# Optimization experiments

Measured on AMD Instinct MI355X. Metric: run time of the kernel, lower is better.

Reference implementation:

```python
import jax, jax.numpy as jnp
import numpy as np

B, N, E, H, F = 4, 10000, 100000, 8, 32
FIN = H * F  # num_in_features == H*F so skip connection is identity add


def setup_inputs() -> dict:
    key = jax.random.key(0)
    ks = jax.random.split(key, 6)
    x = jax.random.normal(ks[0], (B, N, FIN), jnp.float32)
    edge_index = jax.random.randint(ks[1], (B, 2, E), 0, N)
    rel = jax.random.normal(ks[2], (B, E, FIN), jnp.float32)
    W_proj = jax.random.normal(ks[3], (FIN, FIN), jnp.float32) / np.sqrt(FIN).astype(np.float32)
    a_src = jax.random.normal(ks[4], (1, H, F), jnp.float32) * 0.1
    a_trg = jax.random.normal(ks[5], (1, H, F), jnp.float32) * 0.1
    bias = jnp.zeros((FIN,), jnp.float32)
    return dict(x=x, edge_index=edge_index, rel=rel, W_proj=W_proj,
                a_src=a_src, a_trg=a_trg, bias=bias)


def reference(x, edge_index, rel, W_proj, a_src, a_trg, bias):
    # projection: [B,N,FIN] @ [FIN,FIN]^T -> [B,N,H,F]
    proj = (x @ W_proj.T).reshape(B, N, H, F)
    s_src = (proj * a_src).sum(-1)  # [B,N,H]
    s_trg = (proj * a_trg).sum(-1)  # [B,N,H]
    src, trg = edge_index[:, 0], edge_index[:, 1]  # [B,E] each

    gather = jax.vmap(lambda a, i: a[i])  # per-batch index_select along node dim

    # edge lift + leaky relu score: [B,E,H]
    s_e = jax.nn.leaky_relu(gather(s_src, src) + gather(s_trg, trg), negative_slope=0.2)
    # original subtracts the GLOBAL max per batch (over flattened E*H)
    s_e = s_e - s_e.reshape(B, -1).max(axis=-1)[:, None, None]
    exp_s = jnp.exp(s_e)

    # scatter softmax denominator over target-node neighborhoods
    seg_sum = jax.vmap(lambda s, t: jax.ops.segment_sum(s, t, num_segments=N))
    denom = seg_sum(exp_s, trg)               # [B,N,H]
    att = exp_s / (gather(denom, trg) + 1e-16)  # [B,E,H]

    # weighted messages + relation features projected with the same linear
    rel_proj = (rel @ W_proj.T).reshape(B, E, H, F)
    msg = gather(proj, src) * att[..., None] + rel_proj  # [B,E,H,F]

    # scatter-add aggregation to target nodes
    out = seg_sum(msg, trg)                   # [B,N,H,F]

    # skip connection (identity because FIN == H*F), concat heads, bias, ELU
    out = out + x.reshape(B, N, H, F)
    out = out.reshape(B, N, H * F) + bias
    return jax.nn.elu(out)
```

## Files before the change

kernel.cpp:

```cpp
#include <hip/hip_runtime.h>

#define B_ 4
#define N_ 10000
#define E_ 100000
#define H_ 8
#define F_ 32
#define FIN_ 256
#define M_ (B_*N_)
#define BE_ (B_*E_)

__device__ __forceinline__ unsigned enc_f(float f){
  unsigned u = __float_as_uint(f);
  return (u & 0x80000000u) ? ~u : (u | 0x80000000u);
}
__device__ __forceinline__ float dec_f(unsigned e){
  return (e & 0x80000000u) ? __uint_as_float(e & 0x7FFFFFFFu)
                           : __uint_as_float(~e);
}

template<int MODE>
__global__ __launch_bounds__(256)
void gemm_k(const float* __restrict__ A, const float* __restrict__ W,
            float* __restrict__ C,
            const float* __restrict__ add1, const float* __restrict__ add2,
            const float* __restrict__ bias)
{
  __shared__ float As[16][132];
  __shared__ float Bs[16][132];
  const int tid  = threadIdx.x;
  const int row0 = blockIdx.x * 128;
  const int col0 = blockIdx.y * 128;
  const int lr   = tid >> 2;
  const int lc4  = (tid & 3) * 4;
  const int tm   = (tid >> 4) * 8;
  const int tn   = (tid & 15) * 8;

  float acc[8][8];
  #pragma unroll
  for (int i = 0; i < 8; i++)
    #pragma unroll
    for (int j = 0; j < 8; j++) acc[i][j] = 0.f;

  for (int kt = 0; kt < FIN_; kt += 16) {
    #pragma unroll
    for (int half = 0; half < 2; half++) {
      int r = row0 + lr + half * 64;
      float4 v = make_float4(0.f, 0.f, 0.f, 0.f);
      if (r < M_) v = *(const float4*)&A[(size_t)r * FIN_ + kt + lc4];
      As[lc4+0][lr + half*64] = v.x;
      As[lc4+1][lr + half*64] = v.y;
      As[lc4+2][lr + half*64] = v.z;
      As[lc4+3][lr + half*64] = v.w;

      int j = col0 + lr + half * 64;
      float4 w = *(const float4*)&W[(size_t)j * FIN_ + kt + lc4];
      Bs[lc4+0][lr + half*64] = w.x;
      Bs[lc4+1][lr + half*64] = w.y;
      Bs[lc4+2][lr + half*64] = w.z;
      Bs[lc4+3][lr + half*64] = w.w;
    }
    __syncthreads();
    #pragma unroll
    for (int k = 0; k < 16; k++) {
      float a[8], b[8];
      *(float4*)&a[0] = *(const float4*)&As[k][tm];
      *(float4*)&a[4] = *(const float4*)&As[k][tm+4];
      *(float4*)&b[0] = *(const float4*)&Bs[k][tn];
      *(float4*)&b[4] = *(const float4*)&Bs[k][tn+4];
      #pragma unroll
      for (int i = 0; i < 8; i++)
        #pragma unroll
        for (int j = 0; j < 8; j++)
          acc[i][j] = fmaf(a[i], b[j], acc[i][j]);
    }
    __syncthreads();
  }

  #pragma unroll
  for (int i = 0; i < 8; i++) {
    int r = row0 + tm + i;
    if (r >= M_) continue;
    if (MODE == 0) {
      *(float4*)&C[(size_t)r * FIN_ + col0 + tn]     = *(float4*)&acc[i][0];
      *(float4*)&C[(size_t)r * FIN_ + col0 + tn + 4] = *(float4*)&acc[i][4];
    } else {
      #pragma unroll
      for (int j = 0; j < 8; j++) {
        int c = col0 + tn + j;
        float v = acc[i][j] + add1[(size_t)r * FIN_ + c]
                            + add2[(size_t)r * FIN_ + c] + bias[c];
        C[(size_t)r * FIN_ + c] = (v > 0.f) ? v : expm1f(v);
      }
    }
  }
}

__global__ void node_scores_k(const float* __restrict__ proj,
                              const float* __restrict__ a_src,
                              const float* __restrict__ a_trg,
                              float* __restrict__ s_src,
                              float* __restrict__ s_trg)
{
  int i = blockIdx.x * 256 + threadIdx.x;
  if (i >= M_ * H_) return;
  int h = i & 7;
  const float* p  = proj  + (size_t)i * F_;
  const float* as = a_src + h * F_;
  const float* at = a_trg + h * F_;
  float ss = 0.f, st = 0.f;
  #pragma unroll
  for (int f = 0; f < F_; f += 4) {
    float4 pv = *(const float4*)&p[f];
    float4 av = *(const float4*)&as[f];
    float4 tv = *(const float4*)&at[f];
    ss += pv.x*av.x + pv.y*av.y + pv.z*av.z + pv.w*av.w;
    st += pv.x*tv.x + pv.y*tv.y + pv.z*tv.z + pv.w*tv.w;
  }
  s_src[i] = ss;
  s_trg[i] = st;
}

__global__ void edge_scores_k(const int* __restrict__ ei,
                              const float* __restrict__ s_src,
                              const float* __restrict__ s_trg,
                              float* __restrict__ s_e,
                              unsigned* __restrict__ bmax)
{
  __shared__ unsigned smax[B_];
  if (threadIdx.x < B_) smax[threadIdx.x] = 0u;
  __syncthreads();

  int i = blockIdx.x * 256 + threadIdx.x;
  int b = 0;
  if (i < BE_) {
    b = i / E_;
    int e = i - b * E_;
    int src = ei[(size_t)b * 2 * E_ + e];
    int trg = ei[(size_t)b * 2 * E_ + E_ + e];
    const float* ps = s_src + ((size_t)b * N_ + src) * H_;
    const float* pt = s_trg + ((size_t)b * N_ + trg) * H_;
    float4 s0 = *(const float4*)ps,     s1 = *(const float4*)(ps + 4);
    float4 t0 = *(const float4*)pt,     t1 = *(const float4*)(pt + 4);
    float v[8] = { s0.x+t0.x, s0.y+t0.y, s0.z+t0.z, s0.w+t0.w,
                   s1.x+t1.x, s1.y+t1.y, s1.z+t1.z, s1.w+t1.w };
    float lmax = -3.4e38f;
    #pragma unroll
    for (int h = 0; h < 8; h++) {
      v[h] = (v[h] > 0.f) ? v[h] : 0.2f * v[h];
      lmax = fmaxf(lmax, v[h]);
    }
    *(float4*)&s_e[(size_t)i * 8]     = make_float4(v[0], v[1], v[2], v[3]);
    *(float4*)&s_e[(size_t)i * 8 + 4] = make_float4(v[4], v[5], v[6], v[7]);
    atomicMax(&smax[b], enc_f(lmax));
  }
  __syncthreads();
  if (threadIdx.x < B_ && smax[threadIdx.x] != 0u)
    atomicMax(&bmax[threadIdx.x], smax[threadIdx.x]);
}

__global__ void count_k(const int* __restrict__ ei, int* __restrict__ cnt)
{
  int i = blockIdx.x * 256 + threadIdx.x;
  if (i >= BE_) return;
  int b = i / E_, e = i - b * E_;
  int trg = ei[(size_t)b * 2 * E_ + E_ + e];
  atomicAdd(&cnt[b * N_ + trg], 1);
}

__global__ __launch_bounds__(1024)
void scan_k(const int* __restrict__ cnt, int* __restrict__ offs,
            int* __restrict__ cursor)
{
  int b = blockIdx.x;
  __shared__ int sdata[1024];
  __shared__ int carry;
  if (threadIdx.x == 0) carry = 0;
  __syncthreads();
  for (int base = 0; base < N_; base += 1024) {
    int idx = base + threadIdx.x;
    int v = (idx < N_) ? cnt[b * N_ + idx] : 0;
    sdata[threadIdx.x] = v;
    __syncthreads();
    #pragma unroll
    for (int off = 1; off < 1024; off <<= 1) {
      int t = (threadIdx.x >= off) ? sdata[threadIdx.x - off] : 0;
      __syncthreads();
      sdata[threadIdx.x] += t;
      __syncthreads();
    }
    int incl = sdata[threadIdx.x];
    int excl = incl - v + carry;
    if (idx < N_) {
      offs[b * N_ + idx]   = b * E_ + excl;
      cursor[b * N_ + idx] = b * E_ + excl;
    }
    __syncthreads();
    if (threadIdx.x == 1023) carry += incl;
    __syncthreads();
  }
}

__global__ void scatter_k(const int* __restrict__ ei, int* __restrict__ cursor,
                          int2* __restrict__ rec)
{
  int i = blockIdx.x * 256 + threadIdx.x;
  if (i >= BE_) return;
  int b = i / E_, e = i - b * E_;
  int src = ei[(size_t)b * 2 * E_ + e];
  int trg = ei[(size_t)b * 2 * E_ + E_ + e];
  int pos = atomicAdd(&cursor[b * N_ + trg], 1);
  rec[pos] = make_int2(src, i);
}

__global__ __launch_bounds__(256)
void agg_k(const int2* __restrict__ rec, const int* __restrict__ offs,
           const int* __restrict__ cnt, const float* __restrict__ s_e,
           const unsigned* __restrict__ bmax,
           const float* __restrict__ proj, const float* __restrict__ rel,
           float* __restrict__ rel_agg, float* __restrict__ out_acc)
{
  int node = blockIdx.x * 4 + (threadIdx.x >> 6);
  if (node >= M_) return;
  int lane = threadIdx.x & 63;
  int b = node / N_;
  float m = dec_f(bmax[b]);
  int start = offs[node];
  int num   = cnt[node];
  int h = lane >> 3;

  float4 pacc = make_float4(0.f, 0.f, 0.f, 0.f);
  float4 racc = make_float4(0.f, 0.f, 0.f, 0.f);
  float  dacc = 0.f;

  for (int i = 0; i < num; i++) {
    int2 r = rec[start + i];
    int src = r.x;
    int ge  = r.y;
    float ex = expf(s_e[(size_t)ge * 8 + h] - m);
    dacc += ex;
    float4 p = *(const float4*)&proj[((size_t)b * N_ + src) * FIN_ + lane * 4];
    pacc.x += p.x * ex; pacc.y += p.y * ex;
    pacc.z += p.z * ex; pacc.w += p.w * ex;
    float4 rv = *(const float4*)&rel[(size_t)ge * FIN_ + lane * 4];
    racc.x += rv.x; racc.y += rv.y; racc.z += rv.z; racc.w += rv.w;
  }

  float inv = 1.f / (dacc + 1e-16f);
  pacc.x *= inv; pacc.y *= inv; pacc.z *= inv; pacc.w *= inv;
  *(float4*)&out_acc[(size_t)node * FIN_ + lane * 4] = pacc;
  *(float4*)&rel_agg[(size_t)node * FIN_ + lane * 4] = racc;
}

extern "C" void kernel_launch(void* const* d_in, const int* in_sizes, int n_in,
                              void* d_out, int out_size, void* d_ws, size_t ws_size,
                              hipStream_t stream)
{
  const float* x     = (const float*)d_in[0];
  const int*   ei    = (const int*)  d_in[1];
  const float* rel   = (const float*)d_in[2];
  const float* W     = (const float*)d_in[3];
  const float* a_src = (const float*)d_in[4];
  const float* a_trg = (const float*)d_in[5];
  const float* bias  = (const float*)d_in[6];
  float* out = (float*)d_out;

  float* ws = (float*)d_ws;
  size_t o = 0;
  float* proj    = ws + o; o += (size_t)M_ * FIN_;
  float* s_src   = ws + o; o += (size_t)M_ * H_;
  float* s_trg   = ws + o; o += (size_t)M_ * H_;
  float* s_e     = ws + o; o += (size_t)BE_ * H_;
  float* rel_agg = ws + o; o += (size_t)M_ * FIN_;
  float* out_acc = ws + o; o += (size_t)M_ * FIN_;
  int* cnt       = (int*)(ws + o);      o += M_;
  unsigned* bmax = (unsigned*)(ws + o); o += B_;
  int* offs      = (int*)(ws + o);      o += M_;
  int* cursor    = (int*)(ws + o);      o += M_;
  if (o & 1) o++;
  int2* rec      = (int2*)(ws + o);     o += (size_t)2 * BE_;

  hipMemsetAsync(cnt, 0, (M_ + B_) * sizeof(int), stream);

  gemm_k<0><<<dim3(313, 2), 256, 0, stream>>>(x, W, proj, nullptr, nullptr, nullptr);

  node_scores_k<<<(M_ * H_ + 255) / 256, 256, 0, stream>>>(proj, a_src, a_trg, s_src, s_trg);

  edge_scores_k<<<(BE_ + 255) / 256, 256, 0, stream>>>(ei, s_src, s_trg, s_e, bmax);

  count_k<<<(BE_ + 255) / 256, 256, 0, stream>>>(ei, cnt);
  scan_k<<<B_, 1024, 0, stream>>>(cnt, offs, cursor);
  scatter_k<<<(BE_ + 255) / 256, 256, 0, stream>>>(ei, cursor, rec);

  agg_k<<<M_ / 4, 256, 0, stream>>>(rec, offs, cnt, s_e, bmax, proj, rel,
                                    rel_agg, out_acc);

  gemm_k<1><<<dim3(313, 2), 256, 0, stream>>>(rel_agg, W, out, out_acc, x, bias);
}
```

Measured before the change: 897.1 us.

## Swizzle GEMM LDS, vectorize epilogue, fuse count, single-block scan, prefetch agg records

```diff
diff --git a/kernel.cpp b/kernel.cpp
--- a/kernel.cpp
+++ b/kernel.cpp
@@ -9,6 +9,8 @@
 #define M_ (B_*N_)
 #define BE_ (B_*E_)
 
+typedef float f4 __attribute__((ext_vector_type(4)));
+
 __device__ __forceinline__ unsigned enc_f(float f){
   unsigned u = __float_as_uint(f);
   return (u & 0x80000000u) ? ~u : (u | 0x80000000u);
@@ -17,6 +19,8 @@
   return (e & 0x80000000u) ? __uint_as_float(e & 0x7FFFFFFFu)
                            : __uint_as_float(~e);
 }
+
+#define SW(c) ((c) + (((c) >> 5) << 1))
 
 template<int MODE>
 __global__ __launch_bounds__(256)
@@ -25,8 +29,8 @@
             const float* __restrict__ add1, const float* __restrict__ add2,
             const float* __restrict__ bias)
 {
-  __shared__ float As[16][132];
-  __shared__ float Bs[16][132];
+  __shared__ float As[16][136];
+  __shared__ float Bs[16][136];
   const int tid  = threadIdx.x;
   const int row0 = blockIdx.x * 128;
   const int col0 = blockIdx.y * 128;
@@ -44,29 +48,30 @@
   for (int kt = 0; kt < FIN_; kt += 16) {
     #pragma unroll
     for (int half = 0; half < 2; half++) {
-      int r = row0 + lr + half * 64;
+      int col = lr + half * 64;
+      int r = row0 + col;
       float4 v = make_float4(0.f, 0.f, 0.f, 0.f);
       if (r < M_) v = *(const float4*)&A[(size_t)r * FIN_ + kt + lc4];
-      As[lc4+0][lr + half*64] = v.x;
-      As[lc4+1][lr + half*64] = v.y;
-      As[lc4+2][lr + half*64] = v.z;
-      As[lc4+3][lr + half*64] = v.w;
-
-      int j = col0 + lr + half * 64;
+      As[lc4+0][SW(col)] = v.x;
+      As[lc4+1][SW(col)] = v.y;
+      As[lc4+2][SW(col)] = v.z;
+      As[lc4+3][SW(col)] = v.w;
+
+      int j = col0 + col;
       float4 w = *(const float4*)&W[(size_t)j * FIN_ + kt + lc4];
-      Bs[lc4+0][lr + half*64] = w.x;
-      Bs[lc4+1][lr + half*64] = w.y;
-      Bs[lc4+2][lr + half*64] = w.z;
-      Bs[lc4+3][lr + half*64] = w.w;
+      Bs[lc4+0][SW(col)] = w.x;
+      Bs[lc4+1][SW(col)] = w.y;
+      Bs[lc4+2][SW(col)] = w.z;
+      Bs[lc4+3][SW(col)] = w.w;
     }
     __syncthreads();
     #pragma unroll
     for (int k = 0; k < 16; k++) {
       float a[8], b[8];
-      *(float4*)&a[0] = *(const float4*)&As[k][tm];
-      *(float4*)&a[4] = *(const float4*)&As[k][tm+4];
-      *(float4*)&b[0] = *(const float4*)&Bs[k][tn];
-      *(float4*)&b[4] = *(const float4*)&Bs[k][tn+4];
+      *(float4*)&a[0] = *(const float4*)&As[k][SW(tm)];
+      *(float4*)&a[4] = *(const float4*)&As[k][SW(tm+4)];
+      *(float4*)&b[0] = *(const float4*)&Bs[k][SW(tn)];
+      *(float4*)&b[4] = *(const float4*)&Bs[k][SW(tn+4)];
       #pragma unroll
       for (int i = 0; i < 8; i++)
         #pragma unroll
@@ -84,12 +89,22 @@
       *(float4*)&C[(size_t)r * FIN_ + col0 + tn]     = *(float4*)&acc[i][0];
       *(float4*)&C[(size_t)r * FIN_ + col0 + tn + 4] = *(float4*)&acc[i][4];
     } else {
+      const size_t ro = (size_t)r * FIN_ + col0 + tn;
       #pragma unroll
-      for (int j = 0; j < 8; j++) {
-        int c = col0 + tn + j;
-        float v = acc[i][j] + add1[(size_t)r * FIN_ + c]
-                            + add2[(size_t)r * FIN_ + c] + bias[c];
-        C[(size_t)r * FIN_ + c] = (v > 0.f) ? v : expm1f(v);
+      for (int q = 0; q < 2; q++) {
+        float4 a1 = *(const float4*)&add1[ro + q*4];
+        float4 a2 = *(const float4*)&add2[ro + q*4];
+        float4 bb = *(const float4*)&bias[col0 + tn + q*4];
+        float vv[4] = { acc[i][q*4+0] + a1.x + a2.x + bb.x,
+                        acc[i][q*4+1] + a1.y + a2.y + bb.y,
+                        acc[i][q*4+2] + a1.z + a2.z + bb.z,
+                        acc[i][q*4+3] + a1.w + a2.w + bb.w };
+        float4 o;
+        o.x = (vv[0] > 0.f) ? vv[0] : expm1f(vv[0]);
+        o.y = (vv[1] > 0.f) ? vv[1] : expm1f(vv[1]);
+        o.z = (vv[2] > 0.f) ? vv[2] : expm1f(vv[2]);
+        o.w = (vv[3] > 0.f) ? vv[3] : expm1f(vv[3]);
+        *(float4*)&C[ro + q*4] = o;
       }
     }
   }
@@ -124,19 +139,20 @@
                               const float* __restrict__ s_src,
                               const float* __restrict__ s_trg,
                               float* __restrict__ s_e,
-                              unsigned* __restrict__ bmax)
+                              unsigned* __restrict__ bmax,
+                              int* __restrict__ cnt)
 {
   __shared__ unsigned smax[B_];
   if (threadIdx.x < B_) smax[threadIdx.x] = 0u;
   __syncthreads();
 
   int i = blockIdx.x * 256 + threadIdx.x;
-  int b = 0;
   if (i < BE_) {
-    b = i / E_;
+    int b = i / E_;
     int e = i - b * E_;
     int src = ei[(size_t)b * 2 * E_ + e];
     int trg = ei[(size_t)b * 2 * E_ + E_ + e];
+    atomicAdd(&cnt[b * N_ + trg], 1);
     const float* ps = s_src + ((size_t)b * N_ + src) * H_;
     const float* pt = s_trg + ((size_t)b * N_ + trg) * H_;
     float4 s0 = *(const float4*)ps,     s1 = *(const float4*)(ps + 4);
@@ -158,45 +174,43 @@
     atomicMax(&bmax[threadIdx.x], smax[threadIdx.x]);
 }
 
-__global__ void count_k(const int* __restrict__ ei, int* __restrict__ cnt)
-{
-  int i = blockIdx.x * 256 + threadIdx.x;
-  if (i >= BE_) return;
-  int b = i / E_, e = i - b * E_;
-  int trg = ei[(size_t)b * 2 * E_ + E_ + e];
-  atomicAdd(&cnt[b * N_ + trg], 1);
-}
-
 __global__ __launch_bounds__(1024)
 void scan_k(const int* __restrict__ cnt, int* __restrict__ offs,
             int* __restrict__ cursor)
 {
-  int b = blockIdx.x;
-  __shared__ int sdata[1024];
-  __shared__ int carry;
-  if (threadIdx.x == 0) carry = 0;
+  const int PER = 40;
+  int t = threadIdx.x;
+  int lane = t & 63, wid = t >> 6;
+  int base = t * PER;
+
+  int pre[PER];
+  int s = 0;
+  #pragma unroll
+  for (int i = 0; i < PER; i++) {
+    int idx = base + i;
+    int v = (idx < M_) ? cnt[idx] : 0;
+    pre[i] = s; s += v;
+  }
+  int incl = s;
+  #pragma unroll
+  for (int off = 1; off < 64; off <<= 1) {
+    int n = __shfl_up(incl, off);
+    if (lane >= off) incl += n;
+  }
+  __shared__ int wtot[16];
+  if (lane == 63) wtot[wid] = incl;
   __syncthreads();
-  for (int base = 0; base < N_; base += 1024) {
-    int idx = base + threadIdx.x;
-    int v = (idx < N_) ? cnt[b * N_ + idx] : 0;
-    sdata[threadIdx.x] = v;
-    __syncthreads();
-    #pragma unroll
-    for (int off = 1; off < 1024; off <<= 1) {
-      int t = (threadIdx.x >= off) ? sdata[threadIdx.x - off] : 0;
-      __syncthreads();
-      sdata[threadIdx.x] += t;
-      __syncthreads();
-    }
-    int incl = sdata[threadIdx.x];
-    int excl = incl - v + carry;
-    if (idx < N_) {
-      offs[b * N_ + idx]   = b * E_ + excl;
-      cursor[b * N_ + idx] = b * E_ + excl;
-    }
-    __syncthreads();
-    if (threadIdx.x == 1023) carry += incl;
-    __syncthreads();
+  int wbase = 0;
+  for (int w = 0; w < wid; w++) wbase += wtot[w];
+  int tp = wbase + (incl - s);
+  #pragma unroll
+  for (int i = 0; i < PER; i++) {
+    int idx = base + i;
+    if (idx < M_) {
+      int o = tp + pre[i];
+      offs[idx] = o;
+      cursor[idx] = o;
+    }
   }
 }
 
@@ -228,27 +242,29 @@
   int num   = cnt[node];
   int h = lane >> 3;
 
-  float4 pacc = make_float4(0.f, 0.f, 0.f, 0.f);
-  float4 racc = make_float4(0.f, 0.f, 0.f, 0.f);
-  float  dacc = 0.f;
-
-  for (int i = 0; i < num; i++) {
-    int2 r = rec[start + i];
-    int src = r.x;
-    int ge  = r.y;
-    float ex = expf(s_e[(size_t)ge * 8 + h] - m);
-    dacc += ex;
-    float4 p = *(const float4*)&proj[((size_t)b * N_ + src) * FIN_ + lane * 4];
-    pacc.x += p.x * ex; pacc.y += p.y * ex;
-    pacc.z += p.z * ex; pacc.w += p.w * ex;
-    float4 rv = *(const float4*)&rel[(size_t)ge * FIN_ + lane * 4];
-    racc.x += rv.x; racc.y += rv.y; racc.z += rv.z; racc.w += rv.w;
+  f4 pacc = (f4)(0.f);
+  f4 racc = (f4)(0.f);
+  float dacc = 0.f;
+
+  if (num > 0) {
+    int2 cur = rec[start];
+    for (int i = 0; i < num; i++) {
+      int2 nxt = (i + 1 < num) ? rec[start + i + 1] : cur;
+      float ex = expf(s_e[(size_t)cur.y * 8 + h] - m);
+      f4 p  = *(const f4*)&proj[((size_t)b * N_ + cur.x) * FIN_ + lane * 4];
+      f4 rv = __builtin_nontemporal_load(
+                (const f4*)&rel[(size_t)cur.y * FIN_ + lane * 4]);
+      dacc += ex;
+      pacc += p * ex;
+      racc += rv;
+      cur = nxt;
+    }
   }
 
   float inv = 1.f / (dacc + 1e-16f);
-  pacc.x *= inv; pacc.y *= inv; pacc.z *= inv; pacc.w *= inv;
-  *(float4*)&out_acc[(size_t)node * FIN_ + lane * 4] = pacc;
-  *(float4*)&rel_agg[(size_t)node * FIN_ + lane * 4] = racc;
+  pacc *= inv;
+  *(f4*)&out_acc[(size_t)node * FIN_ + lane * 4] = pacc;
+  *(f4*)&rel_agg[(size_t)node * FIN_ + lane * 4] = racc;
 }
 
 extern "C" void kernel_launch(void* const* d_in, const int* in_sizes, int n_in,
@@ -285,10 +301,10 @@
 
   node_scores_k<<<(M_ * H_ + 255) / 256, 256, 0, stream>>>(proj, a_src, a_trg, s_src, s_trg);
 
-  edge_scores_k<<<(BE_ + 255) / 256, 256, 0, stream>>>(ei, s_src, s_trg, s_e, bmax);
-
-  count_k<<<(BE_ + 255) / 256, 256, 0, stream>>>(ei, cnt);
-  scan_k<<<B_, 1024, 0, stream>>>(cnt, offs, cursor);
+  edge_scores_k<<<(BE_ + 255) / 256, 256, 0, stream>>>(ei, s_src, s_trg, s_e, bmax, cnt);
+
+  scan_k<<<1, 1024, 0, stream>>>(cnt, offs, cursor);
+
   scatter_k<<<(BE_ + 255) / 256, 256, 0, stream>>>(ei, cursor, rec);
 
   agg_k<<<M_ / 4, 256, 0, stream>>>(rec, offs, cnt, s_e, bmax, proj, rel,
```

Result: no change. 889.3 us (-0.9%).
